# Optimization experiments

Hardware: AMD Instinct MI355X
Metric: run time of the kernel (lower is better)

The kernel has to match this reference:

```python
import jax, jax.numpy as jnp
import numpy as np
import math

B, S = 512, 100
L, U = 50000, 2000
D, LOC_DIM, USER_DIM, TEMP_DIM = 80, 56, 12, 12
NHEAD, DFF = 4, 160


def _pe(seq_len, d):
    pos = np.arange(seq_len, dtype=np.float32)[:, None]
    div = np.exp(np.arange(0, d, 2, dtype=np.float32) * (-math.log(10000.0) / d))
    pe = np.zeros((seq_len, d), dtype=np.float32)
    pe[:, 0::2] = np.sin(pos * div)
    pe[:, 1::2] = np.cos(pos * div)
    return jnp.asarray(pe)


def _ln(x, g, b, eps=1e-5):
    m = x.mean(-1, keepdims=True)
    v = ((x - m) ** 2).mean(-1, keepdims=True)
    return (x - m) * jax.lax.rsqrt(v + eps) * g + b


def setup_inputs():
    key = jax.random.key(0)
    ks = jax.random.split(key, 16)
    f32 = jnp.float32
    def n(k, shape, s):
        return (jax.random.normal(k, shape) * s).astype(f32)
    return {
        'loc_seq': jax.random.randint(ks[0], (B, S), 0, L),
        'user_seq': jax.random.randint(ks[1], (B, S), 0, U),
        'weekday_seq': jax.random.randint(ks[2], (B, S), 0, 7),
        'start_min_seq': (jax.random.uniform(ks[3], (B, S)) * 1440.0).astype(f32),
        'dur_seq': (jax.random.uniform(ks[4], (B, S)) * 120.0).astype(f32),
        'diff_seq': jax.random.randint(ks[5], (B, S), 0, 7),
        'mask': jnp.ones((B, S), dtype=bool),
        'loc_emb': n(ks[6], (L, LOC_DIM), 0.01).at[0].set(0.0),
        'user_emb': n(ks[7], (U, USER_DIM), 0.01).at[0].set(0.0),
        'Wt': n(ks[8], (6, TEMP_DIM), 0.3), 'bt': jnp.zeros((TEMP_DIM,), f32),
        'in_g': jnp.ones((D,), f32), 'in_b': jnp.zeros((D,), f32),
        'Wq': n(ks[9], (D, D), 0.05), 'bq': jnp.zeros((D,), f32),
        'Wk': n(ks[10], (D, D), 0.05), 'bk': jnp.zeros((D,), f32),
        'Wv': n(ks[11], (D, D), 0.05), 'bv': jnp.zeros((D,), f32),
        'Wo': n(ks[12], (D, D), 0.05), 'bo': jnp.zeros((D,), f32),
        'ln1_g': jnp.ones((D,), f32), 'ln1_b': jnp.zeros((D,), f32),
        'W1': n(ks[13], (D, DFF), 0.05), 'b1': jnp.zeros((DFF,), f32),
        'W2': n(ks[14], (DFF, D), 0.05), 'b2': jnp.zeros((D,), f32),
        'ln2_g': jnp.ones((D,), f32), 'ln2_b': jnp.zeros((D,), f32),
        'out_g': jnp.ones((D,), f32), 'out_b': jnp.zeros((D,), f32),
        'Wp': n(ks[15], (D, L), 0.05), 'bp': jnp.zeros((L,), f32),
        'recency_decay': jnp.array(0.62, f32),
        'freq_weight': jnp.array(2.2, f32),
        'history_scale': jnp.array(11.0, f32),
        'model_weight': jnp.array(0.22, f32),
    }


def reference(loc_seq, user_seq, weekday_seq, start_min_seq, dur_seq, diff_seq, mask,
              loc_emb, user_emb, Wt, bt, in_g, in_b,
              Wq, bq, Wk, bk, Wv, bv, Wo, bo, ln1_g, ln1_b,
              W1, b1, W2, b2, ln2_g, ln2_b, out_g, out_b, Wp, bp,
              recency_decay, freq_weight, history_scale, model_weight):
    b, s = loc_seq.shape
    nloc = Wp.shape[1]
    valid = mask.astype(jnp.float32)
    # --- history scores: the torch per-timestep scatter loop, vectorized ---
    t = jnp.arange(s)
    rec_w = recency_decay ** (s - 1 - t).astype(jnp.float32)      # (s,) decay^time_from_end
    bidx = jnp.broadcast_to(jnp.arange(b)[:, None], (b, s))
    recency = jnp.zeros((b, nloc), jnp.float32).at[bidx, loc_seq].max(rec_w[None, :] * valid)
    freq = jnp.zeros((b, nloc), jnp.float32).at[bidx, loc_seq].add(valid)
    freq = freq / jnp.maximum(freq.max(axis=1, keepdims=True), 1.0)
    history_scores = history_scale * (recency + freq_weight * freq)
    # --- embeddings & temporal features ---
    time_rad = start_min_seq / 60.0 / 24.0 * 2.0 * math.pi
    wd_rad = weekday_seq.astype(jnp.float32) / 7.0 * 2.0 * math.pi
    feats = jnp.stack([jnp.sin(time_rad), jnp.cos(time_rad), jnp.log1p(dur_seq) / 8.0,
                       jnp.sin(wd_rad), jnp.cos(wd_rad), diff_seq.astype(jnp.float32) / 7.0], axis=-1)
    x = jnp.concatenate([loc_emb[loc_seq], user_emb[user_seq], feats @ Wt + bt], axis=-1)
    x = _ln(x, in_g, in_b) + _pe(s, x.shape[-1])[None]
    # --- 1-layer post-norm transformer encoder, erf-gelu, eval (no dropout) ---
    dh = D // NHEAD
    q = (x @ Wq + bq).reshape(b, s, NHEAD, dh)
    k = (x @ Wk + bk).reshape(b, s, NHEAD, dh)
    v = (x @ Wv + bv).reshape(b, s, NHEAD, dh)
    scores = jnp.einsum('bqhd,bkhd->bhqk', q, k) / math.sqrt(dh)
    scores = jnp.where(mask[:, None, None, :], scores, -1e9)
    attn = jnp.einsum('bhqk,bkhd->bqhd', jax.nn.softmax(scores, axis=-1), v).reshape(b, s, D)
    x = _ln(x + attn @ Wo + bo, ln1_g, ln1_b)
    x = _ln(x + jax.nn.gelu(x @ W1 + b1, approximate=False) @ W2 + b2, ln2_g, ln2_b)
    # --- gather last valid position ---
    last_idx = mask.sum(axis=1) - 1
    last = jnp.take_along_axis(x, last_idx[:, None, None], axis=1)[:, 0]
    last = _ln(last, out_g, out_b)
    learned = jax.nn.softmax(last @ Wp + bp, axis=1) * nloc
    return history_scores + model_weight * learned
```

## Files before the change

kernel.cpp:

```cpp
#include <hip/hip_runtime.h>
#include <hip/hip_bf16.h>
#include <math.h>

#define B 512
#define S 100
#define L 50000
#define D 80
#define NHEAD 4
#define DH 20
#define DFF 160
#define NTOK (B*S)
#define NTILES 3125

typedef __attribute__((ext_vector_type(8))) short bf16x8v;
typedef __attribute__((ext_vector_type(4))) float f32x4v;
typedef __attribute__((ext_vector_type(4))) unsigned short u16x4;

__device__ __forceinline__ unsigned short f2bf(float f) {
    unsigned int x = __float_as_uint(f);
    unsigned int r = (x + 0x7FFFu + ((x >> 16) & 1u)) >> 16;
    return (unsigned short)r;
}

__device__ __forceinline__ float pe_val(int s, int d) {
    int k = d >> 1;
    float ang = (float)s * expf(-0.23025850929940458f * (float)k);
    return (d & 1) ? cosf(ang) : sinf(ang);
}

__global__ __launch_bounds__(256) void pack_all(const float* __restrict__ Wq, const float* __restrict__ Wk,
                        const float* __restrict__ Wv, const float* __restrict__ Wo,
                        const float* __restrict__ W1, const float* __restrict__ W2,
                        unsigned short* __restrict__ U) {
    int bid = blockIdx.x;
    const float* W; int K, N, KT, nt; unsigned short* dst;
    if (bid < 15)      { int mt = bid / 5; nt = bid % 5; W = (mt==0)?Wq:(mt==1)?Wk:Wv; K=80; N=80; KT=3; dst = U + (size_t)bid * 1536; }
    else if (bid < 20) { nt = bid - 15; W = Wo; K=80;  N=80;  KT=3; dst = U + 23040 + (size_t)nt * 1536; }
    else if (bid < 30) { nt = bid - 20; W = W1; K=80;  N=160; KT=3; dst = U + 30720 + (size_t)nt * 1536; }
    else               { nt = bid - 30; W = W2; K=160; N=80;  KT=5; dst = U + 46080 + (size_t)nt * 2560; }
    int total = KT * 512;
    for (int idx = threadIdx.x; idx < total; idx += 256) {
        int j = idx & 7, n = (idx >> 3) & 15, q = (idx >> 7) & 3, kt = idx >> 9;
        int k = kt * 32 + q * 8 + j;
        float val = (k < K) ? W[(size_t)k * N + nt * 16 + n] : 0.f;
        dst[idx] = f2bf(val);
    }
}

__global__ __launch_bounds__(256) void build_x(const int* __restrict__ loc_seq, const int* __restrict__ user_seq,
                        const int* __restrict__ weekday_seq, const float* __restrict__ start_min,
                        const float* __restrict__ dur, const int* __restrict__ diff,
                        const float* __restrict__ loc_emb, const float* __restrict__ user_emb,
                        const float* __restrict__ Wt, const float* __restrict__ bt,
                        const float* __restrict__ in_g, const float* __restrict__ in_b,
                        float* __restrict__ x) {
    int token = blockIdx.x * 4 + (threadIdx.x >> 6);
    int lane = threadIdx.x & 63;
    int s = token % S;
    int lidx = loc_seq[token];
    int uidx = user_seq[token];
    float tr = start_min[token] * (2.f * (float)M_PI / 1440.f);
    float wd = (float)weekday_seq[token] * (2.f * (float)M_PI / 7.f);
    float f0 = sinf(tr), f1 = cosf(tr);
    float f2 = log1pf(dur[token]) * 0.125f;
    float f3 = sinf(wd), f4 = cosf(wd);
    float f5 = (float)diff[token] * (1.f / 7.f);
    float v1;
    if (lane < 56) v1 = loc_emb[(size_t)lidx * 56 + lane];
    else           v1 = user_emb[(size_t)uidx * 12 + (lane - 56)];
    float v2 = 0.f;
    if (lane < 4) {
        v2 = user_emb[(size_t)uidx * 12 + 8 + lane];
    } else if (lane < 16) {
        int j = lane - 4;
        v2 = bt[j] + f0 * Wt[j] + f1 * Wt[12 + j] + f2 * Wt[24 + j]
                   + f3 * Wt[36 + j] + f4 * Wt[48 + j] + f5 * Wt[60 + j];
    }
    float sum = v1 + v2, sq = v1 * v1 + v2 * v2;
    #pragma unroll
    for (int off = 1; off < 64; off <<= 1) {
        sum += __shfl_xor(sum, off);
        sq  += __shfl_xor(sq,  off);
    }
    float mean = sum * 0.0125f;
    float var = sq * 0.0125f - mean * mean;
    float rstd = rsqrtf(var + 1e-5f);
    x[(size_t)token * D + lane] = (v1 - mean) * rstd * in_g[lane] + in_b[lane] + pe_val(s, lane);
    if (lane < 16) {
        int d2 = 64 + lane;
        x[(size_t)token * D + d2] = (v2 - mean) * rstd * in_g[d2] + in_b[d2] + pe_val(s, d2);
    }
}

__global__ __launch_bounds__(256) void qkv_attn_fused(const float* __restrict__ x,
      const unsigned short* __restrict__ qkvP,
      const float* __restrict__ bq, const float* __restrict__ bk, const float* __restrict__ bv,
      unsigned short* __restrict__ ao) {
    __shared__ __align__(16) unsigned short qls[128 * 128];
    __shared__ __align__(16) unsigned short kls[112 * 128];
    __shared__ __align__(16) unsigned short vt[4 * 32 * 128];
    __shared__ __align__(16) unsigned short pqk[128 * 128];
    int tid = threadIdx.x;
    int b = blockIdx.x;
    unsigned short* xbf = pqk;
    size_t base = (size_t)b * (S * D);
    f32x4v zz = {0.f, 0.f, 0.f, 0.f};
    f32x4v* q4 = (f32x4v*)qls; f32x4v* k4 = (f32x4v*)kls; f32x4v* v4 = (f32x4v*)vt;
    #pragma unroll
    for (int ii = 0; ii < 8; ++ii) q4[tid + ii * 256] = zz;
    #pragma unroll
    for (int ii = 0; ii < 7; ++ii) k4[tid + ii * 256] = zz;
    #pragma unroll
    for (int ii = 0; ii < 8; ++ii) v4[tid + ii * 256] = zz;
    #pragma unroll
    for (int ii = 0; ii < 8; ++ii) {
        int i = tid + ii * 256;
        if (i < 2000) {
            int row = i / 20, c0 = (i % 20) * 4;
            f32x4v v = *(const f32x4v*)&x[base + row * 80 + c0];
            u16x4 p; p.x = f2bf(v[0]); p.y = f2bf(v[1]); p.z = f2bf(v[2]); p.w = f2bf(v[3]);
            *(u16x4*)&xbf[row * 96 + c0] = p;
        }
    }
    unsigned int* xb32 = (unsigned int*)xbf;
    for (int i = tid; i < 576; i += 256) xb32[4800 + i] = 0;
    for (int i = tid; i < 800; i += 256) { int r = i / 8, c = i % 8; xb32[r * 48 + 40 + c] = 0; }
    __syncthreads();
    int w = tid >> 6, lane = tid & 63;
    int qd = lane >> 4, m = lane & 15;
    for (int mt = w; mt < 7; mt += 4) {
        bf16x8v a[3];
        #pragma unroll
        for (int t = 0; t < 3; ++t)
            a[t] = *(const bf16x8v*)&xbf[(mt * 16 + m) * 96 + t * 32 + qd * 8];
        #pragma unroll
        for (int nt = 0; nt < 15; ++nt) {
            f32x4v acc = {0.f, 0.f, 0.f, 0.f};
            #pragma unroll
            for (int t = 0; t < 3; ++t) {
                bf16x8v bb = *(const bf16x8v*)&qkvP[(((size_t)(nt * 3 + t)) * 4 + qd) * 128 + m * 8];
                acc = __builtin_amdgcn_mfma_f32_16x16x32_bf16(a[t], bb, acc, 0, 0, 0);
            }
            int mat = nt / 5;
            int col80 = nt * 16 + m - mat * 80;
            int h = col80 / 20, dd = col80 % 20;
            const float* bias = (mat == 0) ? bq : (mat == 1) ? bk : bv;
            float bbv = bias[col80];
            float scl = (mat == 0) ? 0.22360679774997896f : 1.f;
            #pragma unroll
            for (int r = 0; r < 4; ++r) {
                int row = mt * 16 + qd * 4 + r;
                unsigned short val = f2bf((acc[r] + bbv) * scl);
                if (mat == 0)      qls[row * 128 + ((h * 32 + dd) ^ ((row & 7) << 3))] = val;
                else if (mat == 1) kls[row * 128 + ((h * 32 + dd) ^ ((row & 7) << 3))] = val;
                else               vt[h * 4096 + dd * 128 + (row ^ ((dd & 7) << 3))] = val;
            }
        }
    }
    __syncthreads();
    #pragma unroll
    for (int ii = 0; ii < 2; ++ii) {
        int i = tid + ii * 256;
        int row = i >> 2, j = (i & 3) * 4;
        u16x4 zp = {0, 0, 0, 0};
        *(u16x4*)&pqk[row * 128 + ((112 + j) ^ ((row & 7) << 3))] = zp;
    }
    #pragma unroll 1
    for (int h = 0; h < 4; ++h) {
        int hb = h * 32;
        bf16x8v aq[2];
        #pragma unroll
        for (int mt2 = 0; mt2 < 2; ++mt2) {
            int row = (w * 2 + mt2) * 16 + m;
            aq[mt2] = *(const bf16x8v*)&qls[row * 128 + ((hb + qd * 8) ^ ((row & 7) << 3))];
        }
        f32x4v sc[2][7];
        #pragma unroll
        for (int nt = 0; nt < 7; ++nt) {
            int krow = nt * 16 + m;
            bf16x8v bk_ = *(const bf16x8v*)&kls[krow * 128 + ((hb + qd * 8) ^ ((krow & 7) << 3))];
            #pragma unroll
            for (int mt2 = 0; mt2 < 2; ++mt2) {
                f32x4v z = {0.f, 0.f, 0.f, 0.f};
                sc[mt2][nt] = __builtin_amdgcn_mfma_f32_16x16x32_bf16(aq[mt2], bk_, z, 0, 0, 0);
            }
        }
        float inv_l[2][4];
        #pragma unroll
        for (int mt2 = 0; mt2 < 2; ++mt2) {
            #pragma unroll
            for (int r = 0; r < 4; ++r) {
                float mx = sc[mt2][0][r];
                #pragma unroll
                for (int nt = 1; nt < 6; ++nt) mx = fmaxf(mx, sc[mt2][nt][r]);
                float s6 = sc[mt2][6][r];
                if (m < 4) mx = fmaxf(mx, s6);
                #pragma unroll
                for (int off = 1; off < 16; off <<= 1) mx = fmaxf(mx, __shfl_xor(mx, off));
                float l = 0.f;
                #pragma unroll
                for (int nt = 0; nt < 6; ++nt) {
                    float p = expf(sc[mt2][nt][r] - mx);
                    sc[mt2][nt][r] = p; l += p;
                }
                float p6 = (m < 4) ? expf(s6 - mx) : 0.f;
                sc[mt2][6][r] = p6; l += p6;
                #pragma unroll
                for (int off = 1; off < 16; off <<= 1) l += __shfl_xor(l, off);
                inv_l[mt2][r] = 1.f / l;
            }
        }
        __syncthreads();
        #pragma unroll
        for (int mt2 = 0; mt2 < 2; ++mt2) {
            #pragma unroll
            for (int r = 0; r < 4; ++r) {
                int row = (w * 2 + mt2) * 16 + qd * 4 + r;
                int sw = (row & 7) << 3;
                #pragma unroll
                for (int nt = 0; nt < 7; ++nt)
                    pqk[row * 128 + ((nt * 16 + m) ^ sw)] = f2bf(sc[mt2][nt][r]);
            }
        }
        __syncthreads();
        f32x4v o[2][2];
        #pragma unroll
        for (int mt2 = 0; mt2 < 2; ++mt2)
            #pragma unroll
            for (int nt2 = 0; nt2 < 2; ++nt2) { f32x4v z = {0.f,0.f,0.f,0.f}; o[mt2][nt2] = z; }
        #pragma unroll
        for (int kt = 0; kt < 4; ++kt) {
            int ksw = (m & 7) << 3;
            bf16x8v bv0 = *(const bf16x8v*)&vt[h * 4096 + (m) * 128 + ((kt * 32 + qd * 8) ^ ksw)];
            bf16x8v bv1 = *(const bf16x8v*)&vt[h * 4096 + (16 + m) * 128 + ((kt * 32 + qd * 8) ^ ksw)];
            #pragma unroll
            for (int mt2 = 0; mt2 < 2; ++mt2) {
                int row = (w * 2 + mt2) * 16 + m;
                bf16x8v pa = *(const bf16x8v*)&pqk[row * 128 + ((kt * 32 + qd * 8) ^ ksw)];
                o[mt2][0] = __builtin_amdgcn_mfma_f32_16x16x32_bf16(pa, bv0, o[mt2][0], 0, 0, 0);
                o[mt2][1] = __builtin_amdgcn_mfma_f32_16x16x32_bf16(pa, bv1, o[mt2][1], 0, 0, 0);
            }
        }
        #pragma unroll
        for (int mt2 = 0; mt2 < 2; ++mt2) {
            #pragma unroll
            for (int r = 0; r < 4; ++r) {
                int srow = (w * 2 + mt2) * 16 + qd * 4 + r;
                if (srow < S) {
                    float iv = inv_l[mt2][r];
                    unsigned short* aop = ao + ((size_t)b * S + srow) * D + h * DH;
                    aop[m] = f2bf(o[mt2][0][r] * iv);
                    if (m < 4) aop[16 + m] = f2bf(o[mt2][1][r] * iv);
                }
            }
        }
    }
}

__global__ __launch_bounds__(256) void encoder_tail(const unsigned short* __restrict__ aog,
      const float* __restrict__ x,
      const unsigned short* __restrict__ woP, const float* __restrict__ bo,
      const float* __restrict__ ln1g, const float* __restrict__ ln1b,
      const unsigned short* __restrict__ w1P, const float* __restrict__ b1,
      const unsigned short* __restrict__ w2P, const float* __restrict__ b2,
      const float* __restrict__ ln2g, const float* __restrict__ ln2b,
      const float* __restrict__ outg, const float* __restrict__ outb,
      unsigned short* __restrict__ apack) {
    __shared__ unsigned short ubuf[64 * 160];
    __shared__ unsigned short xbf[64 * 96];
    __shared__ float ys[64 * 84];
    __shared__ float rsum[64][4], rsq[64][4];
    __shared__ float mstat[64], rstat[64];
    int tid = threadIdx.x;
    size_t base = (size_t)blockIdx.x * 64 * D;
    #pragma unroll
    for (int ii = 0; ii < 5; ++ii) {
        int i = tid + ii * 256;
        int row = i / 20, c0 = (i % 20) * 4;
        *(u16x4*)&ubuf[row * 96 + c0] = *(const u16x4*)&aog[base + row * 80 + c0];
        *(f32x4v*)&ys[row * 84 + c0] = *(const f32x4v*)&x[base + row * 80 + c0];
    }
    #pragma unroll
    for (int ii = 0; ii < 2; ++ii) {
        int i = tid + ii * 256;
        int row = i >> 3, c = i & 7;
        ((unsigned int*)ubuf)[row * 48 + 40 + c] = 0;
    }
    __syncthreads();
    int w = tid >> 6, lane = tid & 63;
    int qd = lane >> 4, m = lane & 15;
    {
        bf16x8v a[3];
        #pragma unroll
        for (int t = 0; t < 3; ++t)
            a[t] = *(const bf16x8v*)&ubuf[(w * 16 + m) * 96 + t * 32 + qd * 8];
        #pragma unroll
        for (int nt = 0; nt < 5; ++nt) {
            f32x4v acc = {0.f, 0.f, 0.f, 0.f};
            #pragma unroll
            for (int t = 0; t < 3; ++t) {
                bf16x8v b = *(const bf16x8v*)&woP[(((size_t)(nt * 3 + t)) * 4 + qd) * 128 + m * 8];
                acc = __builtin_amdgcn_mfma_f32_16x16x32_bf16(a[t], b, acc, 0, 0, 0);
            }
            int col = nt * 16 + m;
            float bbv = bo[col];
            #pragma unroll
            for (int r = 0; r < 4; ++r)
                ys[(w * 16 + qd * 4 + r) * 84 + col] += acc[r] + bbv;
        }
    }
    __syncthreads();
    {
        int row = tid >> 2, qq = tid & 3;
        float s = 0.f, sq = 0.f;
        #pragma unroll
        for (int j = 0; j < 20; ++j) { float v = ys[row * 84 + qq + 4 * j]; s += v; sq += v * v; }
        rsum[row][qq] = s; rsq[row][qq] = sq;
    }
    __syncthreads();
    if (tid < 64) {
        float s = rsum[tid][0] + rsum[tid][1] + rsum[tid][2] + rsum[tid][3];
        float sq = rsq[tid][0] + rsq[tid][1] + rsq[tid][2] + rsq[tid][3];
        float mean = s * 0.0125f;
        float var = sq * 0.0125f - mean * mean;
        mstat[tid] = mean; rstat[tid] = rsqrtf(var + 1e-5f);
    }
    __syncthreads();
    for (int idx = tid; idx < 64 * 96; idx += 256) {
        int row = idx / 96, kk = idx % 96;
        float val = 0.f;
        if (kk < D) {
            val = (ys[row * 84 + kk] - mstat[row]) * rstat[row] * ln1g[kk] + ln1b[kk];
            ys[row * 84 + kk] = val;
        }
        xbf[idx] = f2bf(val);
    }
    __syncthreads();
    {
        bf16x8v a[3];
        #pragma unroll
        for (int t = 0; t < 3; ++t)
            a[t] = *(const bf16x8v*)&xbf[(w * 16 + m) * 96 + t * 32 + qd * 8];
        #pragma unroll
        for (int nt = 0; nt < 10; ++nt) {
            f32x4v acc = {0.f, 0.f, 0.f, 0.f};
            #pragma unroll
            for (int t = 0; t < 3; ++t) {
                bf16x8v b = *(const bf16x8v*)&w1P[(((size_t)(nt * 3 + t)) * 4 + qd) * 128 + m * 8];
                acc = __builtin_amdgcn_mfma_f32_16x16x32_bf16(a[t], b, acc, 0, 0, 0);
            }
            int col = nt * 16 + m;
            float bbv = b1[col];
            #pragma unroll
            for (int r = 0; r < 4; ++r) {
                float aa = acc[r] + bbv;
                float gl = 0.5f * aa * (1.f + erff(aa * 0.70710678118654752f));
                ubuf[(w * 16 + qd * 4 + r) * 160 + col] = f2bf(gl);
            }
        }
    }
    __syncthreads();
    {
        bf16x8v a2[5];
        #pragma unroll
        for (int t = 0; t < 5; ++t)
            a2[t] = *(const bf16x8v*)&ubuf[(w * 16 + m) * 160 + t * 32 + qd * 8];
        #pragma unroll
        for (int nt = 0; nt < 5; ++nt) {
            f32x4v acc = {0.f, 0.f, 0.f, 0.f};
            #pragma unroll
            for (int t = 0; t < 5; ++t) {
                bf16x8v b = *(const bf16x8v*)&w2P[(((size_t)(nt * 5 + t)) * 4 + qd) * 128 + m * 8];
                acc = __builtin_amdgcn_mfma_f32_16x16x32_bf16(a2[t], b, acc, 0, 0, 0);
            }
            int col = nt * 16 + m;
            float bbv = b2[col];
            #pragma unroll
            for (int r = 0; r < 4; ++r)
                ys[(w * 16 + qd * 4 + r) * 84 + col] += acc[r] + bbv;
        }
    }
    __syncthreads();
    {
        int row = tid >> 2, qq = tid & 3;
        float s = 0.f, sq = 0.f;
        #pragma unroll
        for (int j = 0; j < 20; ++j) { float v = ys[row * 84 + qq + 4 * j]; s += v; sq += v * v; }
        rsum[row][qq] = s; rsq[row][qq] = sq;
    }
    __syncthreads();
    if (tid < 64) {
        float s = rsum[tid][0] + rsum[tid][1] + rsum[tid][2] + rsum[tid][3];
        float sq = rsq[tid][0] + rsq[tid][1] + rsq[tid][2] + rsq[tid][3];
        float mean = s * 0.0125f;
        float var = sq * 0.0125f - mean * mean;
        mstat[tid] = mean; rstat[tid] = rsqrtf(var + 1e-5f);
    }
    __syncthreads();
    int t0 = blockIdx.x * 64;
    int srow = (99 - (t0 % 100)) % 100;
    if (srow < 64) {
        float* lastrow = (float*)rsum;
        if (tid < 80)
            lastrow[tid] = (ys[srow * 84 + tid] - mstat[srow]) * rstat[srow] * ln2g[tid] + ln2b[tid];
        __syncthreads();
        if (tid < 64) {
            float v1 = lastrow[tid];
            float v2 = (tid < 16) ? lastrow[64 + tid] : 0.f;
            float sum = v1 + v2, sq = v1 * v1 + v2 * v2;
            #pragma unroll
            for (int off = 1; off < 64; off <<= 1) {
                sum += __shfl_xor(sum, off);
                sq  += __shfl_xor(sq,  off);
            }
            float mean = sum * 0.0125f;
            float var = sq * 0.0125f - mean * mean;
            float rstd = rsqrtf(var + 1e-5f);
            int bb = (t0 + srow) / 100;
            int mtile = bb >> 4, mm = bb & 15;
            {
                int d = tid;
                float val = (v1 - mean) * rstd * outg[d] + outb[d];
                int t = d >> 5, q = (d & 31) >> 3, j = d & 7;
                apack[((((size_t)mtile * 3 + t) * 4 + q) * 16 + mm) * 8 + j] = f2bf(val);
            }
            if (tid < 32) {
                int d = 64 + tid;
                float val = (tid < 16) ? ((v2 - mean) * rstd * outg[d] + outb[d]) : 0.f;
                int t = d >> 5, q = (d & 31) >> 3, j = d & 7;
                apack[((((size_t)mtile * 3 + t) * 4 + q) * 16 + mm) * 8 + j] = f2bf(val);
            }
        }
    }
}

__global__ __launch_bounds__(256) void wp_pack(const float* __restrict__ Wp, unsigned short* __restrict__ bpack,
                                               float* __restrict__ rowsum) {
    int tid = threadIdx.x;
    int nt = blockIdx.x;
    if (nt == 0) { rowsum[tid] = 0.f; rowsum[256 + tid] = 0.f; }
    for (int idx = tid; idx < 1536; idx += 256) {
        int n = idx & 15, kk = idx >> 4;
        int t = kk >> 5, q = (kk & 31) >> 3, j = kk & 7;
        float val = (kk < D) ? Wp[(size_t)kk * L + nt * 16 + n] : 0.f;
        bpack[((((size_t)nt * 3 + t) * 4 + q) * 16 + n) * 8 + j] = f2bf(val);
    }
}

__global__ __launch_bounds__(256) void rowsum_mfma(const unsigned short* __restrict__ apack,
                                                   const unsigned short* __restrict__ bpack,
                                                   const float* __restrict__ bp,
                                                   float* __restrict__ rowsum) {
    __shared__ float part[4][512];
    int tid = threadIdx.x;
    int w = tid >> 6, lane = tid & 63;
    int q = lane >> 4, m = lane & 15;
    int nt0 = (blockIdx.x * 4 + w) * 4;
    const bf16x8v* BP = (const bf16x8v*)bpack;
    const bf16x8v* AP = (const bf16x8v*)apack;
    bf16x8v bfr[4][3];
    float bpv[4], liv[4];
    #pragma unroll
    for (int i = 0; i < 4; ++i) {
        int ntile = nt0 + i;
        int ntc = ntile < NTILES ? ntile : NTILES - 1;
        liv[i] = ntile < NTILES ? 1.f : 0.f;
        #pragma unroll
        for (int t = 0; t < 3; ++t)
            bfr[i][t] = BP[((size_t)ntc * 3 + t) * 64 + q * 16 + m];
        bpv[i] = bp[ntc * 16 + m];
    }
    for (int mt = 0; mt < 32; ++mt) {
        bf16x8v a[3];
        #pragma unroll
        for (int t = 0; t < 3; ++t) a[t] = AP[((size_t)mt * 3 + t) * 64 + q * 16 + m];
        float rs[4] = {0.f, 0.f, 0.f, 0.f};
        #pragma unroll
        for (int i = 0; i < 4; ++i) {
            f32x4v acc = {0.f, 0.f, 0.f, 0.f};
            #pragma unroll
            for (int t = 0; t < 3; ++t)
                acc = __builtin_amdgcn_mfma_f32_16x16x32_bf16(a[t], bfr[i][t], acc, 0, 0, 0);
            #pragma unroll
            for (int r = 0; r < 4; ++r) rs[r] += liv[i] * expf(acc[r] + bpv[i]);
        }
        #pragma unroll
        for (int r = 0; r < 4; ++r) {
            #pragma unroll
            for (int off = 1; off < 16; off <<= 1) rs[r] += __shfl_xor(rs[r], off);
        }
        if (m == 0) {
            #pragma unroll
            for (int r = 0; r < 4; ++r) part[w][mt * 16 + q * 4 + r] = rs[r];
        }
    }
    __syncthreads();
    for (int i = tid; i < 512; i += 256) {
        float s = part[0][i] + part[1][i] + part[2][i] + part[3][i];
        atomicAdd(&rowsum[i], s);
    }
}

__global__ __launch_bounds__(256) void logits_final(const unsigned short* __restrict__ apack,
      const unsigned short* __restrict__ bpack, const float* __restrict__ bp,
      const float* __restrict__ rowsum, const float* __restrict__ mwp,
      float* __restrict__ out) {
    __shared__ float tile[2][16][68];
    __shared__ float sc[512];
    int tid = threadIdx.x;
    int w = tid >> 6, lane = tid & 63;
    int q = lane >> 4, m = lane & 15;
    float mwL = mwp[0] * (float)L;
    for (int i = tid; i < 512; i += 256) sc[i] = mwL / rowsum[i];
    int ntile = blockIdx.x * 4 + w;
    int ntc = ntile < NTILES ? ntile : NTILES - 1;
    bool live = ntile < NTILES;
    const bf16x8v* BP = (const bf16x8v*)bpack;
    const bf16x8v* AP = (const bf16x8v*)apack;
    bf16x8v bfr[3];
    #pragma unroll
    for (int t = 0; t < 3; ++t) bfr[t] = BP[((size_t)ntc * 3 + t) * 64 + q * 16 + m];
    float bpv = bp[ntc * 16 + m];
    int row = tid >> 4, c4 = tid & 15;
    int gc = blockIdx.x * 64 + c4 * 4;
    bool cok = gc + 4 <= L;
    bf16x8v aC[3], aN[3];
    #pragma unroll
    for (int t = 0; t < 3; ++t) aC[t] = AP[(size_t)t * 64 + q * 16 + m];
    __syncthreads();
    for (int mt = 0; mt < 32; ++mt) {
        if (mt < 31) {
            #pragma unroll
            for (int t = 0; t < 3; ++t) aN[t] = AP[((size_t)(mt + 1) * 3 + t) * 64 + q * 16 + m];
        }
        f32x4v acc = {0.f, 0.f, 0.f, 0.f};
        #pragma unroll
        for (int t = 0; t < 3; ++t)
            acc = __builtin_amdgcn_mfma_f32_16x16x32_bf16(aC[t], bfr[t], acc, 0, 0, 0);
        int buf = mt & 1;
        if (live) {
            #pragma unroll
            for (int r = 0; r < 4; ++r)
                tile[buf][q * 4 + r][w * 16 + m] = expf(acc[r] + bpv);
        }
        __syncthreads();
        if (cok) {
            float4 v = *(float4*)&tile[buf][row][c4 * 4];
            float s = sc[mt * 16 + row];
            v.x *= s; v.y *= s; v.z *= s; v.w *= s;
            *(float4*)&out[(size_t)(mt * 16 + row) * L + gc] = v;
        }
        #pragma unroll
        for (int t = 0; t < 3; ++t) aC[t] = aN[t];
    }
}

__global__ void history_kern(const int* __restrict__ loc_seq, const float* __restrict__ decp,
                             const float* __restrict__ fwp, const float* __restrict__ hsp,
                             float* __restrict__ out) {
    int b = blockIdx.x;
    int t = threadIdx.x;
    __shared__ int locs[S];
    __shared__ float red[128];
    if (t < S) locs[t] = loc_seq[(size_t)b * S + t];
    __syncthreads();
    int cnt = 0;
    bool isLast = false;
    int myloc = -1;
    if (t < S) {
        myloc = locs[t];
        isLast = true;
        for (int u = 0; u < S; ++u) {
            if (locs[u] == myloc) { cnt++; if (u > t) isLast = false; }
        }
    }
    red[t] = (float)cnt;
    __syncthreads();
    for (int off = 64; off; off >>= 1) { if (t < off) red[t] = fmaxf(red[t], red[t + off]); __syncthreads(); }
    float denom = fmaxf(red[0], 1.0f);
    if (t < S && isLast) {
        float rec = powf(decp[0], (float)(S - 1 - t));
        out[(size_t)b * L + myloc] += hsp[0] * (rec + fwp[0] * (float)cnt / denom);
    }
}

extern "C" void kernel_launch(void* const* d_in, const int* in_sizes, int n_in,
                              void* d_out, int out_size, void* d_ws, size_t ws_size,
                              hipStream_t stream) {
    (void)in_sizes; (void)n_in; (void)out_size; (void)ws_size;
    const int*   loc_seq   = (const int*)  d_in[0];
    const int*   user_seq  = (const int*)  d_in[1];
    const int*   weekday   = (const int*)  d_in[2];
    const float* start_min = (const float*)d_in[3];
    const float* dur       = (const float*)d_in[4];
    const int*   diff      = (const int*)  d_in[5];
    const float* loc_emb = (const float*)d_in[7];
    const float* user_emb= (const float*)d_in[8];
    const float* Wt  = (const float*)d_in[9];  const float* bt  = (const float*)d_in[10];
    const float* in_g= (const float*)d_in[11]; const float* in_b= (const float*)d_in[12];
    const float* Wq  = (const float*)d_in[13]; const float* bq  = (const float*)d_in[14];
    const float* Wk  = (const float*)d_in[15]; const float* bk  = (const float*)d_in[16];
    const float* Wv  = (const float*)d_in[17]; const float* bv  = (const float*)d_in[18];
    const float* Wo  = (const float*)d_in[19]; const float* bo  = (const float*)d_in[20];
    const float* ln1g= (const float*)d_in[21]; const float* ln1b= (const float*)d_in[22];
    const float* W1  = (const float*)d_in[23]; const float* b1  = (const float*)d_in[24];
    const float* W2  = (const float*)d_in[25]; const float* b2  = (const float*)d_in[26];
    const float* ln2g= (const float*)d_in[27]; const float* ln2b= (const float*)d_in[28];
    const float* outg= (const float*)d_in[29]; const float* outb= (const float*)d_in[30];
    const float* Wp  = (const float*)d_in[31]; const float* bp  = (const float*)d_in[32];
    const float* dec = (const float*)d_in[33]; const float* fw  = (const float*)d_in[34];
    const float* hs  = (const float*)d_in[35]; const float* mw  = (const float*)d_in[36];

    float* ws   = (float*)d_ws;
    float* X    = ws;
    unsigned short* APACK = (unsigned short*)(ws + 4096000);
    unsigned short* AO = (unsigned short*)(ws + 16384000);
    float* RSUM = ws + 20480000;
    unsigned short* WPACKS = (unsigned short*)(ws + 20481000);
    unsigned short* QKVP = WPACKS;
    unsigned short* WOP  = WPACKS + 23040;
    unsigned short* W1P  = WPACKS + 30720;
    unsigned short* W2P  = WPACKS + 46080;
    unsigned short* BPACK = AO;
    float* out  = (float*)d_out;

    pack_all<<<35, 256, 0, stream>>>(Wq, Wk, Wv, Wo, W1, W2, WPACKS);
    build_x<<<NTOK / 4, 256, 0, stream>>>(loc_seq, user_seq, weekday, start_min, dur, diff,
                                          loc_emb, user_emb, Wt, bt, in_g, in_b, X);
    qkv_attn_fused<<<B, 256, 0, stream>>>(X, QKVP, bq, bk, bv, AO);
    encoder_tail<<<NTOK / 64, 256, 0, stream>>>(AO, X, WOP, bo, ln1g, ln1b,
                                                W1P, b1, W2P, b2, ln2g, ln2b,
                                                outg, outb, APACK);
    wp_pack<<<NTILES, 256, 0, stream>>>(Wp, BPACK, RSUM);
    rowsum_mfma<<<(NTILES + 15) / 16, 256, 0, stream>>>(APACK, BPACK, bp, RSUM);
    logits_final<<<(NTILES + 3) / 4, 256, 0, stream>>>(APACK, BPACK, bp, RSUM, mw, out);
    history_kern<<<B, 128, 0, stream>>>(loc_seq, dec, fw, hs, out);
}
```

Before: 387.4 us.

## Store embedded activations as bf16 and stage attention output through LDS

build_x now writes the normalized input activations as bf16 instead of fp32. This halves the global traffic for that buffer in build_x, qkv_attn_fused and encoder_tail. The attention kernel keeps all four heads' outputs in registers, writes them to shared memory, and then stores them to global memory with coalesced 16-byte vector writes instead of scattered 2-byte stores. The residual path in encoder_tail now reads a bf16-rounded x, which loses some precision, and unrolling the head loop raises register pressure.

Result: no change. 387.1 us (-0.1%).

```diff
diff --git a/kernel.cpp b/kernel.cpp
--- a/kernel.cpp
+++ b/kernel.cpp
@@ -15,11 +15,16 @@
 typedef __attribute__((ext_vector_type(8))) short bf16x8v;
 typedef __attribute__((ext_vector_type(4))) float f32x4v;
 typedef __attribute__((ext_vector_type(4))) unsigned short u16x4;
+typedef __attribute__((ext_vector_type(8))) unsigned short u16x8;
 
 __device__ __forceinline__ unsigned short f2bf(float f) {
     unsigned int x = __float_as_uint(f);
     unsigned int r = (x + 0x7FFFu + ((x >> 16) & 1u)) >> 16;
     return (unsigned short)r;
+}
+
+__device__ __forceinline__ float bf2f(unsigned short u) {
+    return __uint_as_float(((unsigned int)u) << 16);
 }
 
 __device__ __forceinline__ float pe_val(int s, int d) {
@@ -53,7 +58,7 @@
                         const float* __restrict__ loc_emb, const float* __restrict__ user_emb,
                         const float* __restrict__ Wt, const float* __restrict__ bt,
                         const float* __restrict__ in_g, const float* __restrict__ in_b,
-                        float* __restrict__ x) {
+                        unsigned short* __restrict__ x) {
     int token = blockIdx.x * 4 + (threadIdx.x >> 6);
     int lane = threadIdx.x & 63;
     int s = token % S;
@@ -85,14 +90,14 @@
     float mean = sum * 0.0125f;
     float var = sq * 0.0125f - mean * mean;
     float rstd = rsqrtf(var + 1e-5f);
-    x[(size_t)token * D + lane] = (v1 - mean) * rstd * in_g[lane] + in_b[lane] + pe_val(s, lane);
+    x[(size_t)token * D + lane] = f2bf((v1 - mean) * rstd * in_g[lane] + in_b[lane] + pe_val(s, lane));
     if (lane < 16) {
         int d2 = 64 + lane;
-        x[(size_t)token * D + d2] = (v2 - mean) * rstd * in_g[d2] + in_b[d2] + pe_val(s, d2);
-    }
-}
-
-__global__ __launch_bounds__(256) void qkv_attn_fused(const float* __restrict__ x,
+        x[(size_t)token * D + d2] = f2bf((v2 - mean) * rstd * in_g[d2] + in_b[d2] + pe_val(s, d2));
+    }
+}
+
+__global__ __launch_bounds__(256) void qkv_attn_fused(const unsigned short* __restrict__ xg,
       const unsigned short* __restrict__ qkvP,
       const float* __restrict__ bq, const float* __restrict__ bk, const float* __restrict__ bv,
       unsigned short* __restrict__ ao) {
@@ -117,9 +122,7 @@
         int i = tid + ii * 256;
         if (i < 2000) {
             int row = i / 20, c0 = (i % 20) * 4;
-            f32x4v v = *(const f32x4v*)&x[base + row * 80 + c0];
-            u16x4 p; p.x = f2bf(v[0]); p.y = f2bf(v[1]); p.z = f2bf(v[2]); p.w = f2bf(v[3]);
-            *(u16x4*)&xbf[row * 96 + c0] = p;
+            *(u16x4*)&xbf[row * 96 + c0] = *(const u16x4*)&xg[base + row * 80 + c0];
         }
     }
     unsigned int* xb32 = (unsigned int*)xbf;
@@ -165,7 +168,8 @@
         u16x4 zp = {0, 0, 0, 0};
         *(u16x4*)&pqk[row * 128 + ((112 + j) ^ ((row & 7) << 3))] = zp;
     }
-    #pragma unroll 1
+    f32x4v os[4][2][2];
+    #pragma unroll
     for (int h = 0; h < 4; ++h) {
         int hb = h * 32;
         bf16x8v aq[2];
@@ -223,11 +227,10 @@
             }
         }
         __syncthreads();
-        f32x4v o[2][2];
         #pragma unroll
         for (int mt2 = 0; mt2 < 2; ++mt2)
             #pragma unroll
-            for (int nt2 = 0; nt2 < 2; ++nt2) { f32x4v z = {0.f,0.f,0.f,0.f}; o[mt2][nt2] = z; }
+            for (int nt2 = 0; nt2 < 2; ++nt2) { f32x4v z = {0.f,0.f,0.f,0.f}; os[h][mt2][nt2] = z; }
         #pragma unroll
         for (int kt = 0; kt < 4; ++kt) {
             int ksw = (m & 7) << 3;
@@ -237,28 +240,45 @@
             for (int mt2 = 0; mt2 < 2; ++mt2) {
                 int row = (w * 2 + mt2) * 16 + m;
                 bf16x8v pa = *(const bf16x8v*)&pqk[row * 128 + ((kt * 32 + qd * 8) ^ ksw)];
-                o[mt2][0] = __builtin_amdgcn_mfma_f32_16x16x32_bf16(pa, bv0, o[mt2][0], 0, 0, 0);
-                o[mt2][1] = __builtin_amdgcn_mfma_f32_16x16x32_bf16(pa, bv1, o[mt2][1], 0, 0, 0);
-            }
-        }
+                os[h][mt2][0] = __builtin_amdgcn_mfma_f32_16x16x32_bf16(pa, bv0, os[h][mt2][0], 0, 0, 0);
+                os[h][mt2][1] = __builtin_amdgcn_mfma_f32_16x16x32_bf16(pa, bv1, os[h][mt2][1], 0, 0, 0);
+            }
+        }
+        #pragma unroll
+        for (int mt2 = 0; mt2 < 2; ++mt2)
+            #pragma unroll
+            for (int r = 0; r < 4; ++r) {
+                os[h][mt2][0][r] *= inv_l[mt2][r];
+                os[h][mt2][1][r] *= inv_l[mt2][r];
+            }
+    }
+    __syncthreads();
+    unsigned short* aols = pqk;
+    #pragma unroll
+    for (int h = 0; h < 4; ++h) {
         #pragma unroll
         for (int mt2 = 0; mt2 < 2; ++mt2) {
             #pragma unroll
             for (int r = 0; r < 4; ++r) {
-                int srow = (w * 2 + mt2) * 16 + qd * 4 + r;
-                if (srow < S) {
-                    float iv = inv_l[mt2][r];
-                    unsigned short* aop = ao + ((size_t)b * S + srow) * D + h * DH;
-                    aop[m] = f2bf(o[mt2][0][r] * iv);
-                    if (m < 4) aop[16 + m] = f2bf(o[mt2][1][r] * iv);
-                }
-            }
+                int row = (w * 2 + mt2) * 16 + qd * 4 + r;
+                aols[row * 96 + h * 20 + m] = f2bf(os[h][mt2][0][r]);
+                if (m < 4) aols[row * 96 + h * 20 + 16 + m] = f2bf(os[h][mt2][1][r]);
+            }
+        }
+    }
+    __syncthreads();
+    #pragma unroll
+    for (int ii = 0; ii < 4; ++ii) {
+        int i = tid + ii * 256;
+        if (i < 1000) {
+            int row = i / 10, c = (i % 10) * 8;
+            *(u16x8*)&ao[base + row * 80 + c] = *(u16x8*)&aols[row * 96 + c];
         }
     }
 }
 
 __global__ __launch_bounds__(256) void encoder_tail(const unsigned short* __restrict__ aog,
-      const float* __restrict__ x,
+      const unsigned short* __restrict__ xg,
       const unsigned short* __restrict__ woP, const float* __restrict__ bo,
       const float* __restrict__ ln1g, const float* __restrict__ ln1b,
       const unsigned short* __restrict__ w1P, const float* __restrict__ b1,
@@ -278,7 +298,11 @@
         int i = tid + ii * 256;
         int row = i / 20, c0 = (i % 20) * 4;
         *(u16x4*)&ubuf[row * 96 + c0] = *(const u16x4*)&aog[base + row * 80 + c0];
-        *(f32x4v*)&ys[row * 84 + c0] = *(const f32x4v*)&x[base + row * 80 + c0];
+        u16x4 xv = *(const u16x4*)&xg[base + row * 80 + c0];
+        f32x4v xf;
+        #pragma unroll
+        for (int j = 0; j < 4; ++j) xf[j] = bf2f(xv[j]);
+        *(f32x4v*)&ys[row * 84 + c0] = xf;
     }
     #pragma unroll
     for (int ii = 0; ii < 2; ++ii) {
@@ -612,7 +636,7 @@
     const float* hs  = (const float*)d_in[35]; const float* mw  = (const float*)d_in[36];
 
     float* ws   = (float*)d_ws;
-    float* X    = ws;
+    unsigned short* Xb = (unsigned short*)ws;
     unsigned short* APACK = (unsigned short*)(ws + 4096000);
     unsigned short* AO = (unsigned short*)(ws + 16384000);
     float* RSUM = ws + 20480000;
@@ -626,9 +650,9 @@
 
     pack_all<<<35, 256, 0, stream>>>(Wq, Wk, Wv, Wo, W1, W2, WPACKS);
     build_x<<<NTOK / 4, 256, 0, stream>>>(loc_seq, user_seq, weekday, start_min, dur, diff,
-                                          loc_emb, user_emb, Wt, bt, in_g, in_b, X);
-    qkv_attn_fused<<<B, 256, 0, stream>>>(X, QKVP, bq, bk, bv, AO);
-    encoder_tail<<<NTOK / 64, 256, 0, stream>>>(AO, X, WOP, bo, ln1g, ln1b,
+                                          loc_emb, user_emb, Wt, bt, in_g, in_b, Xb);
+    qkv_attn_fused<<<B, 256, 0, stream>>>(Xb, QKVP, bq, bk, bv, AO);
+    encoder_tail<<<NTOK / 64, 256, 0, stream>>>(AO, Xb, WOP, bo, ln1g, ln1b,
                                                 W1P, b1, W2P, b2, ln2g, ln2b,
                                                 outg, outb, APACK);
     wp_pack<<<NTILES, 256, 0, stream>>>(Wp, BPACK, RSUM);
```
